# Performance work log

Measured on AMD Instinct MI355X. Metric: run time of the kernel, lower is better.

The kernel has to match this reference:

```python
import math
import jax, jax.numpy as jnp
import numpy as np

N, M, DK, DV = 4096, 4096, 512, 512

def setup_inputs() -> dict:
    key = jax.random.key(0)
    k1, k2, k3, k4, k5 = jax.random.split(key, 5)
    return {
        "query": jax.random.normal(k1, (1, N, DK), dtype=jnp.float32),
        "q_k":   jax.random.normal(k2, (1, N, DK), dtype=jnp.float32),
        "q_v":   jax.random.normal(k3, (1, N, DV), dtype=jnp.float32),
        "key":   jax.random.normal(k4, (1, M, DK), dtype=jnp.float32),
        "value": jax.random.normal(k5, (1, M, DV), dtype=jnp.float32),
    }

def reference(query, q_k, q_v, key, value):
    dk = query.shape[-1]
    # diagonal of query[0] @ q_k[0].T without materializing the NxN product
    q_att = jnp.einsum('nd,nd->n', query[0], q_k[0])[:, None]      # [N, 1]
    scores = query[0] @ key[0].T                                    # [N, M]
    scores = jnp.concatenate([scores, q_att], axis=-1)[None]        # [1, N, M+1]
    scores = scores / math.sqrt(dk + 1)
    attention = jax.nn.softmax(scores, axis=-1)                     # [1, N, M+1]
    res = attention[:, :, :-1] @ value                              # [1, N, DV]
    return q_v * q_att + res
```

## Files before the change

### kernel.cpp

```cpp
#include <hip/hip_runtime.h>

#define NQ 4096
#define MK 4096
#define DKC 512
#define DVC 512
#define SCALE 0.044151079f

typedef __attribute__((ext_vector_type(8))) short short8;
typedef __attribute__((ext_vector_type(4))) float f32x4;

__device__ __forceinline__ unsigned short f2bf(float x) {
  unsigned u = __float_as_uint(x);
  u += 0x7fffu + ((u >> 16) & 1u);
  return (unsigned short)(u >> 16);
}
__device__ __forceinline__ float bf2f(unsigned short h) {
  return __uint_as_float((unsigned)h << 16);
}

#define GLL16(g, l)                                                        \
  __builtin_amdgcn_global_load_lds(                                        \
      (const __attribute__((address_space(1))) unsigned int*)(g),          \
      (__attribute__((address_space(3))) unsigned int*)(l), 16, 0, 0)

__global__ __launch_bounds__(256) void prep_all(const float* __restrict__ query,
                                                const float* __restrict__ q_k,
                                                const float* __restrict__ key,
                                                const float* __restrict__ value,
                                                unsigned short* __restrict__ Qb,
                                                unsigned short* __restrict__ Kb,
                                                unsigned short* __restrict__ Vt,
                                                float* __restrict__ qatt) {
  int b = blockIdx.x;
  if (b < 1024) {
    int n = b * 4 + (threadIdx.x >> 6);
    int lane = threadIdx.x & 63;
    const float4* qr = (const float4*)(query + (size_t)n * DKC + lane * 8);
    const float4* kr = (const float4*)(q_k + (size_t)n * DKC + lane * 8);
    float4 a0 = qr[0], a1 = qr[1];
    float4 b0 = kr[0], b1 = kr[1];
    float dot = a0.x * b0.x + a0.y * b0.y + a0.z * b0.z + a0.w * b0.w +
                a1.x * b1.x + a1.y * b1.y + a1.z * b1.z + a1.w * b1.w;
    unsigned short h[8] = {f2bf(a0.x * SCALE), f2bf(a0.y * SCALE), f2bf(a0.z * SCALE),
                           f2bf(a0.w * SCALE), f2bf(a1.x * SCALE), f2bf(a1.y * SCALE),
                           f2bf(a1.z * SCALE), f2bf(a1.w * SCALE)};
    *(short8*)(Qb + (size_t)n * DKC + lane * 8) = *(short8*)h;
#pragma unroll
    for (int off = 1; off < 64; off <<= 1) dot += __shfl_xor(dot, off, 64);
    if (lane == 0) qatt[n] = dot;
  } else if (b < 2048) {
    int i = (b - 1024) * 256 + threadIdx.x;
    const float4* src = (const float4*)key + (size_t)i * 2;
    float4 a0 = src[0], a1 = src[1];
    unsigned short h[8] = {f2bf(a0.x), f2bf(a0.y), f2bf(a0.z), f2bf(a0.w),
                           f2bf(a1.x), f2bf(a1.y), f2bf(a1.z), f2bf(a1.w)};
    *(short8*)(Kb + (size_t)i * 8) = *(short8*)h;
  } else {
    __shared__ float t[32][33];
    int bi = b - 2048;
    int tx = threadIdx.x & 31, ty = threadIdx.x >> 5;
    int m0 = (bi & 127) * 32;
    int d0 = (bi >> 7) * 32;
#pragma unroll
    for (int i = 0; i < 4; ++i)
      t[ty + i * 8][tx] = value[(size_t)(m0 + ty + i * 8) * DVC + d0 + tx];
    __syncthreads();
#pragma unroll
    for (int i = 0; i < 4; ++i)
      Vt[(size_t)(d0 + ty + i * 8) * MK + m0 + tx] = f2bf(t[tx][ty + i * 8]);
  }
}

__global__ __launch_bounds__(256, 4) void gemm_s(const unsigned short* __restrict__ Qb,
                                                 const unsigned short* __restrict__ Kb,
                                                 unsigned short* __restrict__ S,
                                                 float* __restrict__ rowsum_part) {
  __shared__ __align__(16) char lds[33792];
  const int tid = threadIdx.x;
  const int wid = tid >> 6, lane = tid & 63, lr = lane & 15, lh = lane >> 4;
  const int wm = wid >> 1, wn = wid & 1;

  int bid = blockIdx.x;
  int swz = (bid & 7) * 128 + (bid >> 3);
  const int tm = swz >> 5, tn = swz & 31;
  const size_t m0 = (size_t)tm * 128, n0 = (size_t)tn * 128;

  f32x4 acc[4][4];
#pragma unroll
  for (int i = 0; i < 4; ++i)
#pragma unroll
    for (int j = 0; j < 4; ++j) acc[i][j] = (f32x4){0.f, 0.f, 0.f, 0.f};

  const char* abase = (const char*)Qb + m0 * 1024;
  const char* bbase = (const char*)Kb + n0 * 1024;

  for (int ks = 0; ks < 8; ++ks) {
    const int kb = ks * 128;
    {
      char* al = lds;
      char* bl = lds + 16384;
#pragma unroll
      for (int s = 0; s < 4; ++s) {
        int obase = wid * 4096 + s * 1024;
        int o = obase + lane * 16;
        int row = o >> 7;
        int colg = ((o >> 4) & 7) ^ (row & 7);
        GLL16(abase + (size_t)row * 1024 + kb + colg * 16, al + obase);
        GLL16(bbase + (size_t)row * 1024 + kb + colg * 16, bl + obase);
      }
    }
    __syncthreads();
#pragma unroll
    for (int kk = 0; kk < 2; ++kk) {
      short8 af[4], bf[4];
#pragma unroll
      for (int i = 0; i < 4; ++i) {
        int ar = wm * 64 + i * 16 + lr;
        af[i] = *(const short8*)(lds + ar * 128 + ((((kk << 2) + lh) ^ (lr & 7)) << 4));
        int br = wn * 64 + i * 16 + lr;
        bf[i] = *(const short8*)(lds + 16384 + br * 128 + ((((kk << 2) + lh) ^ (lr & 7)) << 4));
      }
#pragma unroll
      for (int i = 0; i < 4; ++i)
#pragma unroll
        for (int j = 0; j < 4; ++j)
          acc[i][j] = __builtin_amdgcn_mfma_f32_16x16x32_bf16(af[i], bf[j], acc[i][j], 0, 0, 0);
    }
    __syncthreads();
  }

  unsigned short* sl = (unsigned short*)lds;
  float* rs = (float*)(lds + 32768);
  float rsum[4][4];
#pragma unroll
  for (int i = 0; i < 4; ++i)
#pragma unroll
    for (int r = 0; r < 4; ++r) rsum[i][r] = 0.f;
#pragma unroll
  for (int i = 0; i < 4; ++i)
#pragma unroll
    for (int j = 0; j < 4; ++j)
#pragma unroll
      for (int r = 0; r < 4; ++r) {
        int m = wm * 64 + i * 16 + lh * 4 + r;
        int n = wn * 64 + j * 16 + lr;
        float e = __expf(acc[i][j][r]);
        sl[m * 128 + n] = f2bf(e);
        rsum[i][r] += e;
      }
#pragma unroll
  for (int i = 0; i < 4; ++i)
#pragma unroll
    for (int r = 0; r < 4; ++r) {
      float v = rsum[i][r];
      v += __shfl_xor(v, 1, 64);
      v += __shfl_xor(v, 2, 64);
      v += __shfl_xor(v, 4, 64);
      v += __shfl_xor(v, 8, 64);
      if (lr == 0) rs[wn * 128 + wm * 64 + i * 16 + lh * 4 + r] = v;
    }
  __syncthreads();
  if (tid < 128) rowsum_part[(size_t)tn * NQ + m0 + tid] = rs[tid] + rs[128 + tid];
#pragma unroll
  for (int i = 0; i < 8; ++i) {
    int o = i * 4096 + tid * 16;
    int row = o >> 8, colb = o & 255;
    *(uint4*)((char*)S + (m0 + row) * 8192 + n0 * 2 + colb) = *(const uint4*)((const char*)sl + o);
  }
}

__global__ __launch_bounds__(256, 4) void gemm_o_part(const unsigned short* __restrict__ P,
                                                      const unsigned short* __restrict__ Vt,
                                                      unsigned short* __restrict__ part) {
  __shared__ __align__(16) char lds[32768];
  const int tid = threadIdx.x;
  const int wid = tid >> 6, lane = tid & 63, lr = lane & 15, lh = lane >> 4;
  const int wm = wid >> 1, wn = wid & 1;

  int bid = blockIdx.x;
  int swz = (bid & 7) * 64 + (bid >> 3);
  const int mt = swz >> 4;
  const int nt = (swz >> 2) & 3;
  const int ksl = swz & 3;
  const size_t m0 = (size_t)mt * 128, n0 = (size_t)nt * 128;

  f32x4 acc[4][4];
#pragma unroll
  for (int i = 0; i < 4; ++i)
#pragma unroll
    for (int j = 0; j < 4; ++j) acc[i][j] = (f32x4){0.f, 0.f, 0.f, 0.f};

  const char* abase = (const char*)P + m0 * 8192 + (size_t)ksl * 2048;
  const char* bbase = (const char*)Vt + n0 * 8192 + (size_t)ksl * 2048;

  for (int ks = 0; ks < 16; ++ks) {
    const int kb = ks * 128;
    {
      char* al = lds;
      char* bl = lds + 16384;
#pragma unroll
      for (int s = 0; s < 4; ++s) {
        int obase = wid * 4096 + s * 1024;
        int o = obase + lane * 16;
        int row = o >> 7;
        int colg = ((o >> 4) & 7) ^ (row & 7);
        GLL16(abase + (size_t)row * 8192 + kb + colg * 16, al + obase);
        GLL16(bbase + (size_t)row * 8192 + kb + colg * 16, bl + obase);
      }
    }
    __syncthreads();
#pragma unroll
    for (int kk = 0; kk < 2; ++kk) {
      short8 af[4], bf[4];
#pragma unroll
      for (int i = 0; i < 4; ++i) {
        int ar = wm * 64 + i * 16 + lr;
        af[i] = *(const short8*)(lds + ar * 128 + ((((kk << 2) + lh) ^ (lr & 7)) << 4));
        int br = wn * 64 + i * 16 + lr;
        bf[i] = *(const short8*)(lds + 16384 + br * 128 + ((((kk << 2) + lh) ^ (lr & 7)) << 4));
      }
#pragma unroll
      for (int i = 0; i < 4; ++i)
#pragma unroll
        for (int j = 0; j < 4; ++j)
          acc[i][j] = __builtin_amdgcn_mfma_f32_16x16x32_bf16(af[i], bf[j], acc[i][j], 0, 0, 0);
    }
    __syncthreads();
  }

  unsigned short* sl = (unsigned short*)lds;
#pragma unroll
  for (int i = 0; i < 4; ++i)
#pragma unroll
    for (int j = 0; j < 4; ++j)
#pragma unroll
      for (int r = 0; r < 4; ++r) {
        int m = wm * 64 + i * 16 + lh * 4 + r;
        int n = wn * 64 + j * 16 + lr;
        sl[m * 128 + n] = f2bf(acc[i][j][r]);
      }
  __syncthreads();
  char* pbase = (char*)part + (size_t)ksl * NQ * DVC * 2;
#pragma unroll
  for (int i = 0; i < 8; ++i) {
    int o = i * 4096 + tid * 16;
    int row = o >> 8, colb = o & 255;
    *(uint4*)(pbase + (m0 + row) * 1024 + n0 * 2 + colb) = *(const uint4*)((const char*)sl + o);
  }
}

__global__ __launch_bounds__(256) void row_inv(const float* __restrict__ rowsum_part,
                                               const float* __restrict__ qatt,
                                               float* __restrict__ inv) {
  int n = blockIdx.x * 256 + threadIdx.x;
  float s = 0.f;
#pragma unroll
  for (int tn = 0; tn < 32; ++tn) s += rowsum_part[(size_t)tn * NQ + n];
  inv[n] = 1.0f / (s + __expf(qatt[n] * SCALE));
}

__global__ __launch_bounds__(256) void combine2(const unsigned short* __restrict__ part,
                                                const float* __restrict__ qatt,
                                                const float* __restrict__ inv,
                                                const float* __restrict__ q_v,
                                                float* __restrict__ out) {
  int idx = blockIdx.x * blockDim.x + threadIdx.x;
  int n = idx >> 6;
  int d8 = (idx & 63) * 8;
  float qa = qatt[n];
  float iv = inv[n];
  size_t off = (size_t)n * DVC + d8;
  float r[8] = {0.f, 0.f, 0.f, 0.f, 0.f, 0.f, 0.f, 0.f};
#pragma unroll
  for (int w = 0; w < 4; ++w) {
    short8 po = *(const short8*)(part + (size_t)w * NQ * DVC + off);
#pragma unroll
    for (int j = 0; j < 8; ++j) r[j] += bf2f((unsigned short)po[j]);
  }
  const float4* qv = (const float4*)(q_v + off);
  float4 qv0 = qv[0], qv1 = qv[1];
  float4 o0 = {qv0.x * qa + r[0] * iv, qv0.y * qa + r[1] * iv, qv0.z * qa + r[2] * iv,
               qv0.w * qa + r[3] * iv};
  float4 o1 = {qv1.x * qa + r[4] * iv, qv1.y * qa + r[5] * iv, qv1.z * qa + r[6] * iv,
               qv1.w * qa + r[7] * iv};
  float4* op = (float4*)(out + off);
  op[0] = o0;
  op[1] = o1;
}

extern "C" void kernel_launch(void* const* d_in, const int* in_sizes, int n_in,
                              void* d_out, int out_size, void* d_ws, size_t ws_size,
                              hipStream_t stream) {
  const float* query = (const float*)d_in[0];
  const float* q_k = (const float*)d_in[1];
  const float* q_v = (const float*)d_in[2];
  const float* key = (const float*)d_in[3];
  const float* value = (const float*)d_in[4];
  float* out = (float*)d_out;

  char* ws = (char*)d_ws;
  unsigned short* Qb = (unsigned short*)(ws);
  unsigned short* Kb = (unsigned short*)(ws + (4u << 20));
  unsigned short* Vt = (unsigned short*)(ws + (8u << 20));
  unsigned short* S = (unsigned short*)(ws + (12u << 20));
  float* qatt = (float*)(ws + (44u << 20));
  unsigned short* part = (unsigned short*)(ws + (45u << 20));
  float* rowsum_part = (float*)(ws + (61u << 20));
  float* inv = (float*)(ws + (62u << 20));

  prep_all<<<dim3(4096), dim3(256), 0, stream>>>(query, q_k, key, value, Qb, Kb, Vt, qatt);
  gemm_s<<<dim3(1024), dim3(256), 0, stream>>>(Qb, Kb, S, rowsum_part);
  gemm_o_part<<<dim3(512), dim3(256), 0, stream>>>(S, Vt, part);
  row_inv<<<dim3(16), dim3(256), 0, stream>>>(rowsum_part, qatt, inv);
  combine2<<<dim3(1024), dim3(256), 0, stream>>>(part, qatt, inv, q_v, out);
}
```

Before: 68.94 us.

## Quantize probabilities and V to FP8 for the PV GEMM and fuse row_inv into combine

Stores the exponentiated scores (pre-scaled by 0.25) and the transposed V as FP8 e4m3 via a software converter. The second GEMM then uses fp8 MFMA with half the K-loop iterations and half the bytes of P read and written. The row-inverse kernel is folded into the combine kernel, which rescales by 4 to undo the 0.25 factor. This cuts memory traffic for the large NxM intermediate and one launch, at the cost of FP8 precision loss and an expensive scalar conversion routine in the epilogue and prep kernels.

```diff
diff --git a/kernel.cpp b/kernel.cpp
--- a/kernel.cpp
+++ b/kernel.cpp
@@ -16,6 +16,31 @@
 }
 __device__ __forceinline__ float bf2f(unsigned short h) {
   return __uint_as_float((unsigned)h << 16);
+}
+
+__device__ __forceinline__ unsigned char f2fp8(float x) {
+  if (x >= 448.0f) return 0x7e;
+  if (x < 0.001953125f) return 0;
+  unsigned u = __float_as_uint(x);
+  int e = (int)((u >> 23) & 255) - 127;
+  if (e < -6) {
+    int m = (int)rintf(x * 512.0f);
+    if (m > 7) return 0x08;
+    return (unsigned char)m;
+  }
+  unsigned mant = u & 0x7fffff;
+  unsigned keep = mant >> 20;
+  unsigned rest = mant & 0xfffff;
+  if (rest > 0x80000 || (rest == 0x80000 && (keep & 1))) keep++;
+  int ee = e;
+  if (keep == 8) { keep = 0; ee++; }
+  if (ee > 8 || (ee == 8 && keep == 7)) return 0x7e;
+  return (unsigned char)(((ee + 7) << 3) | keep);
+}
+__device__ __forceinline__ unsigned char f2fp8s(float x) {
+  unsigned char s = 0;
+  if (x < 0.f) { s = 0x80; x = -x; }
+  return s | f2fp8(x);
 }
 
 #define GLL16(g, l)                                                        \
@@ -29,7 +54,7 @@
                                                 const float* __restrict__ value,
                                                 unsigned short* __restrict__ Qb,
                                                 unsigned short* __restrict__ Kb,
-                                                unsigned short* __restrict__ Vt,
+                                                unsigned char* __restrict__ Vt8,
                                                 float* __restrict__ qatt) {
   int b = blockIdx.x;
   if (b < 1024) {
@@ -67,13 +92,13 @@
     __syncthreads();
 #pragma unroll
     for (int i = 0; i < 4; ++i)
-      Vt[(size_t)(d0 + ty + i * 8) * MK + m0 + tx] = f2bf(t[tx][ty + i * 8]);
+      Vt8[(size_t)(d0 + ty + i * 8) * MK + m0 + tx] = f2fp8s(t[tx][ty + i * 8]);
   }
 }
 
 __global__ __launch_bounds__(256, 4) void gemm_s(const unsigned short* __restrict__ Qb,
                                                  const unsigned short* __restrict__ Kb,
-                                                 unsigned short* __restrict__ S,
+                                                 unsigned char* __restrict__ P8,
                                                  float* __restrict__ rowsum_part) {
   __shared__ __align__(16) char lds[33792];
   const int tid = threadIdx.x;
@@ -129,7 +154,7 @@
     __syncthreads();
   }
 
-  unsigned short* sl = (unsigned short*)lds;
+  unsigned char* sl8 = (unsigned char*)lds;
   float* rs = (float*)(lds + 32768);
   float rsum[4][4];
 #pragma unroll
@@ -145,7 +170,7 @@
         int m = wm * 64 + i * 16 + lh * 4 + r;
         int n = wn * 64 + j * 16 + lr;
         float e = __expf(acc[i][j][r]);
-        sl[m * 128 + n] = f2bf(e);
+        sl8[m * 128 + n] = f2fp8(e * 0.25f);
         rsum[i][r] += e;
       }
 #pragma unroll
@@ -162,15 +187,15 @@
   __syncthreads();
   if (tid < 128) rowsum_part[(size_t)tn * NQ + m0 + tid] = rs[tid] + rs[128 + tid];
 #pragma unroll
-  for (int i = 0; i < 8; ++i) {
+  for (int i = 0; i < 4; ++i) {
     int o = i * 4096 + tid * 16;
-    int row = o >> 8, colb = o & 255;
-    *(uint4*)((char*)S + (m0 + row) * 8192 + n0 * 2 + colb) = *(const uint4*)((const char*)sl + o);
-  }
-}
-
-__global__ __launch_bounds__(256, 4) void gemm_o_part(const unsigned short* __restrict__ P,
-                                                      const unsigned short* __restrict__ Vt,
+    int row = o >> 7, col = o & 127;
+    *(uint4*)(P8 + (m0 + row) * (size_t)MK + n0 + col) = *(const uint4*)(sl8 + o);
+  }
+}
+
+__global__ __launch_bounds__(256, 4) void gemm_o_part(const unsigned char* __restrict__ P8,
+                                                      const unsigned char* __restrict__ Vt8,
                                                       unsigned short* __restrict__ part) {
   __shared__ __align__(16) char lds[32768];
   const int tid = threadIdx.x;
@@ -190,10 +215,10 @@
 #pragma unroll
     for (int j = 0; j < 4; ++j) acc[i][j] = (f32x4){0.f, 0.f, 0.f, 0.f};
 
-  const char* abase = (const char*)P + m0 * 8192 + (size_t)ksl * 2048;
-  const char* bbase = (const char*)Vt + n0 * 8192 + (size_t)ksl * 2048;
-
-  for (int ks = 0; ks < 16; ++ks) {
+  const char* abase = (const char*)P8 + m0 * MK + (size_t)ksl * 1024;
+  const char* bbase = (const char*)Vt8 + n0 * MK + (size_t)ksl * 1024;
+
+  for (int ks = 0; ks < 8; ++ks) {
     const int kb = ks * 128;
     {
       char* al = lds;
@@ -204,26 +229,28 @@
         int o = obase + lane * 16;
         int row = o >> 7;
         int colg = ((o >> 4) & 7) ^ (row & 7);
-        GLL16(abase + (size_t)row * 8192 + kb + colg * 16, al + obase);
-        GLL16(bbase + (size_t)row * 8192 + kb + colg * 16, bl + obase);
-      }
-    }
-    __syncthreads();
-#pragma unroll
-    for (int kk = 0; kk < 2; ++kk) {
-      short8 af[4], bf[4];
+        GLL16(abase + (size_t)row * MK + kb + colg * 16, al + obase);
+        GLL16(bbase + (size_t)row * MK + kb + colg * 16, bl + obase);
+      }
+    }
+    __syncthreads();
+#pragma unroll
+    for (int kk = 0; kk < 4; ++kk) {
+      long af[4], bf[4];
 #pragma unroll
       for (int i = 0; i < 4; ++i) {
         int ar = wm * 64 + i * 16 + lr;
-        af[i] = *(const short8*)(lds + ar * 128 + ((((kk << 2) + lh) ^ (lr & 7)) << 4));
+        int g = 2 * kk + (lh >> 1);
+        af[i] = *(const long*)(lds + ar * 128 + ((g ^ (ar & 7)) << 4) + (lh & 1) * 8);
         int br = wn * 64 + i * 16 + lr;
-        bf[i] = *(const short8*)(lds + 16384 + br * 128 + ((((kk << 2) + lh) ^ (lr & 7)) << 4));
+        int gb = 2 * kk + (lh >> 1);
+        bf[i] = *(const long*)(lds + 16384 + br * 128 + ((gb ^ (br & 7)) << 4) + (lh & 1) * 8);
       }
 #pragma unroll
       for (int i = 0; i < 4; ++i)
 #pragma unroll
         for (int j = 0; j < 4; ++j)
-          acc[i][j] = __builtin_amdgcn_mfma_f32_16x16x32_bf16(af[i], bf[j], acc[i][j], 0, 0, 0);
+          acc[i][j] = __builtin_amdgcn_mfma_f32_16x16x32_fp8_fp8(af[i], bf[j], acc[i][j], 0, 0, 0);
     }
     __syncthreads();
   }
@@ -249,40 +276,41 @@
   }
 }
 
-__global__ __launch_bounds__(256) void row_inv(const float* __restrict__ rowsum_part,
-                                               const float* __restrict__ qatt,
-                                               float* __restrict__ inv) {
-  int n = blockIdx.x * 256 + threadIdx.x;
-  float s = 0.f;
-#pragma unroll
-  for (int tn = 0; tn < 32; ++tn) s += rowsum_part[(size_t)tn * NQ + n];
-  inv[n] = 1.0f / (s + __expf(qatt[n] * SCALE));
-}
-
 __global__ __launch_bounds__(256) void combine2(const unsigned short* __restrict__ part,
+                                                const float* __restrict__ rowsum_part,
                                                 const float* __restrict__ qatt,
-                                                const float* __restrict__ inv,
                                                 const float* __restrict__ q_v,
                                                 float* __restrict__ out) {
-  int idx = blockIdx.x * blockDim.x + threadIdx.x;
-  int n = idx >> 6;
-  int d8 = (idx & 63) * 8;
+  __shared__ float inv_s[4];
+  const int b = blockIdx.x;
+  const int t = threadIdx.x;
+  if (t < 128) {
+    int r = t >> 5, p = t & 31;
+    float v = rowsum_part[(size_t)p * NQ + b * 4 + r];
+#pragma unroll
+    for (int off = 1; off < 32; off <<= 1) v += __shfl_xor(v, off, 32);
+    if (p == 0) inv_s[r] = 4.0f / (v + __expf(qatt[b * 4 + r] * SCALE));
+  }
+  __syncthreads();
+  int r = t >> 6;
+  int d8 = (t & 63) * 8;
+  int n = b * 4 + r;
   float qa = qatt[n];
-  float iv = inv[n];
+  float iv = inv_s[r];
   size_t off = (size_t)n * DVC + d8;
-  float r[8] = {0.f, 0.f, 0.f, 0.f, 0.f, 0.f, 0.f, 0.f};
+  float rr[8] = {0.f, 0.f, 0.f, 0.f, 0.f, 0.f, 0.f, 0.f};
 #pragma unroll
   for (int w = 0; w < 4; ++w) {
     short8 po = *(const short8*)(part + (size_t)w * NQ * DVC + off);
 #pragma unroll
-    for (int j = 0; j < 8; ++j) r[j] += bf2f((unsigned short)po[j]);
+    for (int j = 0; j < 8; ++j) rr[j] += bf2f((unsigned short)po[j]);
   }
   const float4* qv = (const float4*)(q_v + off);
   float4 qv0 = qv[0], qv1 = qv[1];
-  float4 o0 = {qv0.x * qa + r[0] * iv, qv0.y * qa + r[1] * iv, qv0.z * qa + r[2] * iv,
-               qv0.w * qa + r[3] * iv};
-  float4 o1 = {qv1.x * qa + r[4] * iv, qv1.y * qa + r[5] * iv, qv1.z * qa + r[6] * iv,
-               qv1.w * qa + r[7] * iv};
+  float4 o0 = {qv0.x * qa + rr[0] * iv, qv0.y * qa + rr[1] * iv, qv0.z * qa + rr[2] * iv,
+               qv0.w * qa + rr[3] * iv};
+  float4 o1 = {qv1.x * qa + rr[4] * iv, qv1.y * qa + rr[5] * iv, qv1.z * qa + rr[6] * iv,
+               qv1.w * qa + rr[7] * iv};
   float4* op = (float4*)(out + off);
   op[0] = o0;
   op[1] = o1;
@@ -301,16 +329,14 @@
   char* ws = (char*)d_ws;
   unsigned short* Qb = (unsigned short*)(ws);
   unsigned short* Kb = (unsigned short*)(ws + (4u << 20));
-  unsigned short* Vt = (unsigned short*)(ws + (8u << 20));
-  unsigned short* S = (unsigned short*)(ws + (12u << 20));
-  float* qatt = (float*)(ws + (44u << 20));
-  unsigned short* part = (unsigned short*)(ws + (45u << 20));
-  float* rowsum_part = (float*)(ws + (61u << 20));
-  float* inv = (float*)(ws + (62u << 20));
-
-  prep_all<<<dim3(4096), dim3(256), 0, stream>>>(query, q_k, key, value, Qb, Kb, Vt, qatt);
-  gemm_s<<<dim3(1024), dim3(256), 0, stream>>>(Qb, Kb, S, rowsum_part);
-  gemm_o_part<<<dim3(512), dim3(256), 0, stream>>>(S, Vt, part);
-  row_inv<<<dim3(16), dim3(256), 0, stream>>>(rowsum_part, qatt, inv);
-  combine2<<<dim3(1024), dim3(256), 0, stream>>>(part, qatt, inv, q_v, out);
-}
+  unsigned char* Vt8 = (unsigned char*)(ws + (8u << 20));
+  unsigned char* P8 = (unsigned char*)(ws + (12u << 20));
+  float* qatt = (float*)(ws + (28u << 20));
+  unsigned short* part = (unsigned short*)(ws + (29u << 20));
+  float* rowsum_part = (float*)(ws + (45u << 20));
+
+  prep_all<<<dim3(4096), dim3(256), 0, stream>>>(query, q_k, key, value, Qb, Kb, Vt8, qatt);
+  gemm_s<<<dim3(1024), dim3(256), 0, stream>>>(Qb, Kb, P8, rowsum_part);
+  gemm_o_part<<<dim3(512), dim3(256), 0, stream>>>(P8, Vt8, part);
+  combine2<<<dim3(1024), dim3(256), 0, stream>>>(part, rowsum_part, qatt, q_v, out);
+}
```

After: 75.79 us. 9.9% more time.
